# Performance work log

Hardware: AMD Instinct MI355X
Metric: run time of the kernel (lower is better)

## Reference

```python
import jax, jax.numpy as jnp
import numpy as np

BN_EPS = 1e-3  # Keras BatchNormalization default epsilon


def lstm_layer(x, h0, c0, W, U, b):
    # x: [B,T,D]; Keras gate order: i, f, g(cell), o
    def step(carry, xt):
        h, c = carry
        z = xt @ W + h @ U + b               # [B,4H]
        i, f, g, o = jnp.split(z, 4, axis=-1)
        c = jax.nn.sigmoid(f) * c + jax.nn.sigmoid(i) * jnp.tanh(g)
        h = jax.nn.sigmoid(o) * jnp.tanh(c)
        return (h, c), h
    (h, c), ys = jax.lax.scan(step, (h0, c0), x.transpose(1, 0, 2))
    return ys.transpose(1, 0, 2), h, c       # [B,T,H], [B,H], [B,H]


def setup_inputs() -> dict:
    key = jax.random.key(0)
    ks = jax.random.split(key, 8)
    B, T, V, D, H = 64, 128, 32000, 256, 1024
    s = 0.05
    return {
        "tokens": jax.random.randint(ks[0], (B, T), 0, V, dtype=jnp.int32),
        "h0": jnp.zeros((B, H), jnp.float32),
        "c0": jnp.zeros((B, H), jnp.float32),
        "emb": jax.random.normal(ks[1], (V, D), jnp.float32) * s,
        "W0": jax.random.normal(ks[2], (D, 4 * H), jnp.float32) * s,
        "U0": jax.random.normal(ks[3], (H, 4 * H), jnp.float32) * s,
        "b0": jnp.zeros((4 * H,), jnp.float32),
        "W1": jax.random.normal(ks[4], (H, 4 * H), jnp.float32) * s,
        "U1": jax.random.normal(ks[5], (H, 4 * H), jnp.float32) * s,
        "b1": jnp.zeros((4 * H,), jnp.float32),
        "gamma": jnp.ones((H,), jnp.float32),
        "beta": jnp.zeros((H,), jnp.float32),
        "mov_mean": jnp.zeros((H,), jnp.float32),
        "mov_var": jnp.ones((H,), jnp.float32),
    }


def reference(tokens, h0, c0, emb, W0, U0, b0, W1, U1, b1, gamma, beta, mov_mean, mov_var):
    x = emb[tokens]                                   # [B,T,D] embedding lookup
    # Original call() feeds the SAME `hidden` as initial state of layer 0,
    # then the (h,c) of layer 0 as initial state of layer 1 — replicate that.
    x, h, c = lstm_layer(x, h0, c0, W0, U0, b0)
    out, h, c = lstm_layer(x, h, c, W1, U1, b1)
    # BatchNormalization at inference (dropout inactive, moving stats used)
    inv = jax.lax.rsqrt(mov_var + BN_EPS)
    norm = (out - mov_mean) * inv * gamma + beta
    return norm, h, c
```

## Files before the change

kernel.cpp:

```cpp
#include <hip/hip_runtime.h>
#include <hip/hip_bf16.h>


typedef __attribute__((ext_vector_type(8))) short short8;
typedef __attribute__((ext_vector_type(4))) short short4v;
typedef __attribute__((ext_vector_type(4))) float f32x4;
typedef __attribute__((ext_vector_type(16))) float f32x16;
typedef unsigned short ushort_t;

__device__ __forceinline__ void lgkm0_bar() {
  asm volatile("s_waitcnt lgkmcnt(0)" ::: "memory");
  __builtin_amdgcn_s_barrier();
}

__device__ __forceinline__ ushort_t f2b(float f) {
  __hip_bfloat16 h = __float2bfloat16(f);
  return *reinterpret_cast<ushort_t*>(&h);
}
__device__ __forceinline__ float b2f(ushort_t u) {
  unsigned int x = ((unsigned int)u) << 16;
  return __builtin_bit_cast(float, x);
}
__device__ __forceinline__ float fsigmoid(float x) {
  return 1.f / (1.f + __expf(-x));
}
__device__ __forceinline__ float ftanh(float x) {
  return 1.f - 2.f / (__expf(2.f * x) + 1.f);
}

__device__ __forceinline__ void gload_lds16(const ushort_t* g, ushort_t* l) {
  __builtin_amdgcn_global_load_lds(
      (const __attribute__((address_space(1))) unsigned int*)g,
      (__attribute__((address_space(3))) unsigned int*)l, 16, 0, 0);
}

__global__ __launch_bounds__(256) void k_convert(
    const float* __restrict__ src, ushort_t* __restrict__ dst, int kshift) {
  size_t tid = (size_t)blockIdx.x * 256 + threadIdx.x;
  int k = (int)(tid >> 12);
  int c = (int)(tid & 4095);
  int pc = ((c & 1023) << 2) | (c >> 10);
  dst[((size_t)pc << kshift) + k] = f2b(src[tid]);
}

__global__ __launch_bounds__(256) void k_convert_u(
    const float* __restrict__ src, ushort_t* __restrict__ dst) {
  int cid = blockIdx.x * 256 + threadIdx.x;
  int l = cid & 63;
  int ks = (cid >> 6) & 15;
  int kh = (cid >> 10) & 3;
  int ws = cid >> 12;
  int pc = ws * 32 + (l & 31);
  int c = ((pc & 3) << 10) | (pc >> 2);
  int k0 = kh * 256 + ks * 16 + (l >> 5) * 8;
  short8 v;
#pragma unroll
  for (int e = 0; e < 8; ++e)
    v[e] = (short)f2b(src[(size_t)(k0 + e) * 4096 + c]);
  *(short8*)(dst + (size_t)cid * 8) = v;
}

__global__ __launch_bounds__(256) void k_bias(
    const float* __restrict__ b0, const float* __restrict__ b1,
    float* __restrict__ bp0, float* __restrict__ bp1) {
  int pc = blockIdx.x * 256 + threadIdx.x;
  int c = ((pc & 3) << 10) | (pc >> 2);
  bp0[pc] = b0[c];
  bp1[pc] = b1[c];
}

__global__ __launch_bounds__(256) void k_gather(
    const int* __restrict__ tokens, const float* __restrict__ emb,
    ushort_t* __restrict__ Xef) {
  int row = blockIdx.x;
  int t = row >> 6, b = row & 63;
  int tok = tokens[b * 128 + t];
  int d = threadIdx.x;
  Xef[(size_t)row * 256 + d] = f2b(emb[(size_t)tok * 256 + d]);
}

__global__ __launch_bounds__(256) void k_init(
    const float* __restrict__ h0, const float* __restrict__ c0,
    ushort_t* __restrict__ hall, float* __restrict__ c_st,
    unsigned* __restrict__ bars) {
  int tid = blockIdx.x * 256 + threadIdx.x;
  c_st[tid] = c0[tid];
  hall[tid] = f2b(h0[tid]);
  if (tid < 512) bars[tid] = 0;
}

template <int NKS, int LAY>
__global__ __launch_bounds__(256) void k_gemm(
    const ushort_t* __restrict__ Af, const ushort_t* __restrict__ BT,
    ushort_t* __restrict__ C) {
  const int K = NKS * 16;
  const int xcd = blockIdx.x & 7, loc = blockIdx.x >> 3;
  const int wgM = xcd * 8 + (loc & 7);
  const int wgN = loc >> 3;
  const int tid = threadIdx.x;
  const int l = tid & 63;
  const int wv = tid >> 6;
  const int wvM = wv & 1, wvN = wv >> 1;

  __shared__ __align__(16) ushort_t Alds[4096];
  __shared__ __align__(16) ushort_t Blds[4096];

  const int m0 = wgM * 128, n0 = wgN * 128;
  f32x4 acc[4][4] = {};

  for (int k0 = 0; k0 < K; k0 += 32) {
    __syncthreads();
#pragma unroll
    for (int jj = 0; jj < 2; ++jj) {
      int c = jj * 256 + tid;
      int kc = c >> 7, r = c & 127;
      int R = m0 + r;
      int kcg = (k0 >> 3) + kc;
      const ushort_t* asrc =
          (LAY == 0) ? (Af + (size_t)R * 256 + kcg * 8)
                     : (Af + (size_t)(R >> 6) * 65536 + (R & 63) * 1024 + kcg * 8);
      gload_lds16(asrc, (ushort_t*)&Alds[(size_t)(jj * 256 + (tid & ~63)) * 8]);
      gload_lds16(BT + (size_t)(n0 + r) * K + k0 + kc * 8,
                  (ushort_t*)&Blds[(size_t)(jj * 256 + (tid & ~63)) * 8]);
    }
    __syncthreads();

    short8 af[4], bf[4];
#pragma unroll
    for (int mt = 0; mt < 4; ++mt)
      af[mt] = *(const short8*)&Alds[((l >> 4) * 128 + wvM * 64 + mt * 16 + (l & 15)) * 8];
#pragma unroll
    for (int nt = 0; nt < 4; ++nt)
      bf[nt] = *(const short8*)&Blds[((l >> 4) * 128 + wvN * 64 + nt * 16 + (l & 15)) * 8];
#pragma unroll
    for (int mt = 0; mt < 4; ++mt)
#pragma unroll
      for (int nt = 0; nt < 4; ++nt)
        acc[mt][nt] =
            __builtin_amdgcn_mfma_f32_16x16x32_bf16(af[mt], bf[nt], acc[mt][nt], 0, 0, 0);
  }

  const int rr0 = wgM * 128 + wvM * 64 + (l >> 4) * 4;
  const int cc0 = wgN * 128 + wvN * 64 + (l & 15);
#pragma unroll
  for (int mt = 0; mt < 4; ++mt)
#pragma unroll
    for (int nt = 0; nt < 4; ++nt)
#pragma unroll
      for (int r = 0; r < 4; ++r)
        C[(size_t)(rr0 + mt * 16 + r) * 4096 + cc0 + nt * 16] =
            f2b(acc[mt][nt][r]);
}

template <int LAYER>
__global__ __launch_bounds__(256, 1) void k_pers(
    const ushort_t* __restrict__ Uf,
    const ushort_t* __restrict__ XW,
    const float* __restrict__ bp,
    ushort_t* __restrict__ hall,
    float* __restrict__ c_st,
    float* __restrict__ outp,
    const float* __restrict__ gamma, const float* __restrict__ beta,
    const float* __restrict__ mean, const float* __restrict__ var,
    unsigned* __restrict__ bar) {
  const int bid = blockIdx.x;
  const int xcd = bid & 7;
  const int g = xcd & 1;
  const int ws = (xcd >> 1) * 32 + (bid >> 3);
  const int tid = threadIdx.x;
  const int l = tid & 63;
  const int kh = tid >> 6;

  __shared__ __align__(16) ushort_t Ulds[32768];
  __shared__ float zls[4][32][33];
  __shared__ ushort_t hbuf[32][8];

  {
    const ushort_t* src = Uf + (size_t)ws * 32768;
    for (int i = tid; i < 4096; i += 256)
      *(short8*)(Ulds + (size_t)i * 8) = *(const short8*)(src + (size_t)i * 8);
  }

  const int row_o = tid & 31, j_o = tid >> 5;
  const int rowg = g * 32 + row_o;
  const int j = ws * 8 + j_o;
  float creg = c_st[rowg * 1024 + j];
  const f32x4 bias_v = *(const f32x4*)(bp + ws * 32 + j_o * 4);
  float scl = 0.f, sft = 0.f;
  if (LAYER == 1) {
    float inv = rsqrtf(var[j] + 1e-3f);
    scl = inv * gamma[j];
    sft = beta[j] - mean[j] * scl;
  }

  unsigned* grp = bar + xcd * 16;
  unsigned* root = bar + 128 + g * 16;
  const bool leader = (bid >> 3) == 0;

  __syncthreads();

#pragma unroll 1
  for (int t = 0; t < 128; ++t) {
    const ushort_t* hin =
        hall + (size_t)((LAYER == 1 && t == 0) ? 128 : t) * 65536;
    ushort_t* hout = hall + (size_t)(t + 1) * 65536;

    const ushort_t* ab =
        hin + (size_t)(g * 32 + (l & 31)) * 1024 + kh * 256 + (l >> 5) * 8;
    short8 ar[16];
#pragma unroll
    for (int ks = 0; ks < 16; ++ks)
      ar[ks] = *(const short8*)(ab + ks * 16);

    short4v xw = *(const short4v*)(
        XW + ((size_t)(t * 64 + rowg) << 12) + ws * 32 + j_o * 4);

    const ushort_t* uB = Ulds + (size_t)kh * 8192;
    f32x16 acc0 = {}, acc1 = {}, acc2 = {}, acc3 = {};
#pragma unroll
    for (int ks = 0; ks < 16; ks += 4) {
      short8 b0 = *(const short8*)(uB + (size_t)(ks + 0) * 512 + l * 8);
      short8 b1 = *(const short8*)(uB + (size_t)(ks + 1) * 512 + l * 8);
      short8 b2 = *(const short8*)(uB + (size_t)(ks + 2) * 512 + l * 8);
      short8 b3 = *(const short8*)(uB + (size_t)(ks + 3) * 512 + l * 8);
      acc0 = __builtin_amdgcn_mfma_f32_32x32x16_bf16(ar[ks + 0], b0, acc0, 0, 0, 0);
      acc1 = __builtin_amdgcn_mfma_f32_32x32x16_bf16(ar[ks + 1], b1, acc1, 0, 0, 0);
      acc2 = __builtin_amdgcn_mfma_f32_32x32x16_bf16(ar[ks + 2], b2, acc2, 0, 0, 0);
      acc3 = __builtin_amdgcn_mfma_f32_32x32x16_bf16(ar[ks + 3], b3, acc3, 0, 0, 0);
    }
    f32x16 zt = (acc0 + acc1) + (acc2 + acc3);

#pragma unroll
    for (int r = 0; r < 16; ++r)
      zls[kh][(r & 3) + 8 * (r >> 2) + 4 * (l >> 5)][l & 31] = zt[r];
    lgkm0_bar();

    float z4[4];
#pragma unroll
    for (int gi = 0; gi < 4; ++gi) {
      int c = j_o * 4 + gi;
      z4[gi] = ((zls[0][row_o][c] + zls[1][row_o][c]) +
                (zls[2][row_o][c] + zls[3][row_o][c])) +
               b2f((ushort_t)xw[gi]) + bias_v[gi];
    }
    float ii = fsigmoid(z4[0]), ff = fsigmoid(z4[1]);
    float gg = ftanh(z4[2]), oo = fsigmoid(z4[3]);
    creg = ff * creg + ii * gg;
    float hn = oo * ftanh(creg);
    hbuf[row_o][j_o] = f2b(hn);
    if (LAYER == 1) {
      outp[((size_t)rowg * 128 + t) * 1024 + j] = hn * scl + sft;
      if (t == 127) {
        outp[8388608 + rowg * 1024 + j] = hn;
        outp[8454144 + rowg * 1024 + j] = creg;
      }
    } else if (t == 127) {
      c_st[rowg * 1024 + j] = creg;
    }
    lgkm0_bar();

    if (tid < 32) {
      short8 v = *(const short8*)&hbuf[tid][0];
      union { short8 s; unsigned u[4]; } cv;
      cv.s = v;
      unsigned* dst = (unsigned*)(hout + (size_t)(g * 32 + tid) * 1024 + ws * 8);
#pragma unroll
      for (int wi = 0; wi < 4; ++wi)
        __hip_atomic_store(dst + wi, cv.u[wi], __ATOMIC_RELAXED,
                           __HIP_MEMORY_SCOPE_AGENT);
    }

    asm volatile("s_waitcnt vmcnt(0)" ::: "memory");
    __builtin_amdgcn_s_barrier();
    if (tid == 0) {
      __hip_atomic_fetch_add(grp, 1u, __ATOMIC_RELAXED,
                             __HIP_MEMORY_SCOPE_AGENT);
      if (leader) {
        unsigned tg = 32u * (unsigned)(t + 1);
        while (__hip_atomic_load(grp, __ATOMIC_RELAXED,
                                 __HIP_MEMORY_SCOPE_AGENT) < tg)
          __builtin_amdgcn_s_sleep(1);
        __hip_atomic_fetch_add(root, 1u, __ATOMIC_RELAXED,
                               __HIP_MEMORY_SCOPE_AGENT);
      }
      unsigned tr = 4u * (unsigned)(t + 1);
      while (__hip_atomic_load(root, __ATOMIC_RELAXED,
                               __HIP_MEMORY_SCOPE_AGENT) < tr)
        __builtin_amdgcn_s_sleep(1);
    }
    __builtin_amdgcn_s_barrier();
  }
}

extern "C" void kernel_launch(void* const* d_in, const int* in_sizes, int n_in,
                              void* d_out, int out_size, void* d_ws,
                              size_t ws_size, hipStream_t stream) {
  const int* tokens = (const int*)d_in[0];
  const float* h0 = (const float*)d_in[1];
  const float* c0 = (const float*)d_in[2];
  const float* emb = (const float*)d_in[3];
  const float* W0 = (const float*)d_in[4];
  const float* U0 = (const float*)d_in[5];
  const float* b0 = (const float*)d_in[6];
  const float* W1 = (const float*)d_in[7];
  const float* U1 = (const float*)d_in[8];
  const float* b1 = (const float*)d_in[9];
  const float* gammap = (const float*)d_in[10];
  const float* betap = (const float*)d_in[11];
  const float* mmean = (const float*)d_in[12];
  const float* mvar = (const float*)d_in[13];

  char* ws = (char*)d_ws;
  ushort_t* Uc0 = (ushort_t*)(ws + 0);
  ushort_t* Uc1 = (ushort_t*)(ws + 8388608);
  ushort_t* W0f = (ushort_t*)(ws + 16777216);
  ushort_t* W1f = (ushort_t*)(ws + 18874368);
  float* bp0 = (float*)(ws + 27262976);
  float* bp1 = (float*)(ws + 27279360);
  ushort_t* Xef = (ushort_t*)(ws + 27295744);
  ushort_t* XW = (ushort_t*)(ws + 31490048);
  ushort_t* hall = (ushort_t*)(ws + 98598912);
  float* c_st = (float*)(ws + 115507200);
  unsigned* bars = (unsigned*)(ws + 115769344);

  k_convert_u<<<2048, 256, 0, stream>>>(U0, Uc0);
  k_convert_u<<<2048, 256, 0, stream>>>(U1, Uc1);
  k_convert<<<4096, 256, 0, stream>>>(W0, W0f, 8);
  k_convert<<<16384, 256, 0, stream>>>(W1, W1f, 10);
  k_bias<<<16, 256, 0, stream>>>(b0, b1, bp0, bp1);
  k_gather<<<8192, 256, 0, stream>>>(tokens, emb, Xef);
  k_init<<<256, 256, 0, stream>>>(h0, c0, hall, c_st, bars);

  float* outp = (float*)d_out;

  k_gemm<16, 0><<<2048, 256, 0, stream>>>(Xef, W0f, XW);
  k_pers<0><<<256, 256, 0, stream>>>(Uc0, XW, bp0, hall, c_st, nullptr,
                                     nullptr, nullptr, nullptr, nullptr,
                                     bars);

  k_gemm<64, 1><<<2048, 256, 0, stream>>>(hall + 65536, W1f, XW);
  k_pers<1><<<256, 256, 0, stream>>>(Uc1, XW, bp1, hall, c_st, outp, gammap,
                                     betap, mmean, mvar, bars + 160);
}
```

Baseline: 1.773 ms.

## Halve persistent LSTM blocks, widen per-block U slice, flatten grid barrier

```diff
diff --git a/kernel.cpp b/kernel.cpp
--- a/kernel.cpp
+++ b/kernel.cpp
@@ -47,12 +47,13 @@
     const float* __restrict__ src, ushort_t* __restrict__ dst) {
   int cid = blockIdx.x * 256 + threadIdx.x;
   int l = cid & 63;
-  int ks = (cid >> 6) & 15;
-  int kh = (cid >> 10) & 3;
-  int ws = cid >> 12;
-  int pc = ws * 32 + (l & 31);
+  int ks = (cid >> 6) & 31;
+  int kh = (cid >> 11) & 1;
+  int nt = (cid >> 12) & 1;
+  int ws = cid >> 13;
+  int pc = ws * 64 + nt * 32 + (l & 31);
   int c = ((pc & 3) << 10) | (pc >> 2);
-  int k0 = kh * 256 + ks * 16 + (l >> 5) * 8;
+  int k0 = kh * 512 + ks * 16 + (l >> 5) * 8;
   short8 v;
 #pragma unroll
   for (int e = 0; e < 8; ++e)
@@ -164,38 +165,41 @@
     const float* __restrict__ mean, const float* __restrict__ var,
     unsigned* __restrict__ bar) {
   const int bid = blockIdx.x;
-  const int xcd = bid & 7;
-  const int g = xcd & 1;
-  const int ws = (xcd >> 1) * 32 + (bid >> 3);
+  const int g = bid & 1;
+  const int ws = bid >> 1;
   const int tid = threadIdx.x;
   const int l = tid & 63;
-  const int kh = tid >> 6;
-
-  __shared__ __align__(16) ushort_t Ulds[32768];
-  __shared__ float zls[4][32][33];
-  __shared__ ushort_t hbuf[32][8];
+  const int wv = tid >> 6;
+  const int nt = wv & 1, kh = wv >> 1;
+
+  __shared__ __align__(16) ushort_t Ulds[65536];
+  __shared__ float zls[2][2][32][33];
+  __shared__ ushort_t hbuf[32][16];
 
   {
-    const ushort_t* src = Uf + (size_t)ws * 32768;
-    for (int i = tid; i < 4096; i += 256)
+    const ushort_t* src = Uf + (size_t)ws * 65536;
+    for (int i = tid; i < 8192; i += 256)
       *(short8*)(Ulds + (size_t)i * 8) = *(const short8*)(src + (size_t)i * 8);
   }
 
-  const int row_o = tid & 31, j_o = tid >> 5;
+  const int row_o = tid & 31, jp = tid >> 5;
   const int rowg = g * 32 + row_o;
-  const int j = ws * 8 + j_o;
-  float creg = c_st[rowg * 1024 + j];
-  const f32x4 bias_v = *(const f32x4*)(bp + ws * 32 + j_o * 4);
-  float scl = 0.f, sft = 0.f;
-  if (LAYER == 1) {
-    float inv = rsqrtf(var[j] + 1e-3f);
-    scl = inv * gamma[j];
-    sft = beta[j] - mean[j] * scl;
+  float creg[2], scl[2], sft[2];
+#pragma unroll
+  for (int q = 0; q < 2; ++q) {
+    int j = ws * 16 + jp * 2 + q;
+    creg[q] = c_st[rowg * 1024 + j];
+    if (LAYER == 1) {
+      float inv = rsqrtf(var[j] + 1e-3f);
+      scl[q] = inv * gamma[j];
+      sft[q] = beta[j] - mean[j] * scl[q];
+    }
   }
-
-  unsigned* grp = bar + xcd * 16;
-  unsigned* root = bar + 128 + g * 16;
-  const bool leader = (bid >> 3) == 0;
+  const f32x4 bias0 = *(const f32x4*)(bp + ws * 64 + jp * 8);
+  const f32x4 bias1 = *(const f32x4*)(bp + ws * 64 + jp * 8 + 4);
+
+  short8 xwn = *(const short8*)(
+      XW + ((size_t)(0 * 64 + rowg) << 12) + ws * 64 + jp * 8);
 
   __syncthreads();
 
@@ -206,19 +210,16 @@
     ushort_t* hout = hall + (size_t)(t + 1) * 65536;
 
     const ushort_t* ab =
-        hin + (size_t)(g * 32 + (l & 31)) * 1024 + kh * 256 + (l >> 5) * 8;
-    short8 ar[16];
-#pragma unroll
-    for (int ks = 0; ks < 16; ++ks)
+        hin + (size_t)(g * 32 + (l & 31)) * 1024 + kh * 512 + (l >> 5) * 8;
+    short8 ar[32];
+#pragma unroll
+    for (int ks = 0; ks < 32; ++ks)
       ar[ks] = *(const short8*)(ab + ks * 16);
 
-    short4v xw = *(const short4v*)(
-        XW + ((size_t)(t * 64 + rowg) << 12) + ws * 32 + j_o * 4);
-
-    const ushort_t* uB = Ulds + (size_t)kh * 8192;
+    const ushort_t* uB = Ulds + (size_t)(nt * 2 + kh) * 16384;
     f32x16 acc0 = {}, acc1 = {}, acc2 = {}, acc3 = {};
 #pragma unroll
-    for (int ks = 0; ks < 16; ks += 4) {
+    for (int ks = 0; ks < 32; ks += 4) {
       short8 b0 = *(const short8*)(uB + (size_t)(ks + 0) * 512 + l * 8);
       short8 b1 = *(const short8*)(uB + (size_t)(ks + 1) * 512 + l * 8);
       short8 b2 = *(const short8*)(uB + (size_t)(ks + 2) * 512 + l * 8);
@@ -232,38 +233,37 @@
 
 #pragma unroll
     for (int r = 0; r < 16; ++r)
-      zls[kh][(r & 3) + 8 * (r >> 2) + 4 * (l >> 5)][l & 31] = zt[r];
+      zls[kh][nt][(r & 3) + 8 * (r >> 2) + 4 * (l >> 5)][l & 31] = zt[r];
     lgkm0_bar();
 
-    float z4[4];
-#pragma unroll
-    for (int gi = 0; gi < 4; ++gi) {
-      int c = j_o * 4 + gi;
-      z4[gi] = ((zls[0][row_o][c] + zls[1][row_o][c]) +
-                (zls[2][row_o][c] + zls[3][row_o][c])) +
-               b2f((ushort_t)xw[gi]) + bias_v[gi];
-    }
-    float ii = fsigmoid(z4[0]), ff = fsigmoid(z4[1]);
-    float gg = ftanh(z4[2]), oo = fsigmoid(z4[3]);
-    creg = ff * creg + ii * gg;
-    float hn = oo * ftanh(creg);
-    hbuf[row_o][j_o] = f2b(hn);
-    if (LAYER == 1) {
-      outp[((size_t)rowg * 128 + t) * 1024 + j] = hn * scl + sft;
-      if (t == 127) {
-        outp[8388608 + rowg * 1024 + j] = hn;
-        outp[8454144 + rowg * 1024 + j] = creg;
-      }
-    } else if (t == 127) {
-      c_st[rowg * 1024 + j] = creg;
+    float hn2[2];
+#pragma unroll
+    for (int q = 0; q < 2; ++q) {
+      const int j_o = jp * 2 + q;
+      const int nte = j_o >> 3;
+      const int cb = (j_o & 7) * 4;
+      f32x4 zv0 = *(const f32x4*)&zls[0][nte][row_o][cb];
+      f32x4 zv1 = *(const f32x4*)&zls[1][nte][row_o][cb];
+      const f32x4& bv = q ? bias1 : bias0;
+      float zi = zv0[0] + zv1[0] + b2f((ushort_t)xwn[q * 4 + 0]) + bv[0];
+      float zf = zv0[1] + zv1[1] + b2f((ushort_t)xwn[q * 4 + 1]) + bv[1];
+      float zg = zv0[2] + zv1[2] + b2f((ushort_t)xwn[q * 4 + 2]) + bv[2];
+      float zo = zv0[3] + zv1[3] + b2f((ushort_t)xwn[q * 4 + 3]) + bv[3];
+      float ii = fsigmoid(zi), ff = fsigmoid(zf), oo = fsigmoid(zo);
+      float gg = ftanh(zg);
+      creg[q] = ff * creg[q] + ii * gg;
+      hn2[q] = oo * ftanh(creg[q]);
+      hbuf[row_o][j_o] = f2b(hn2[q]);
     }
     lgkm0_bar();
 
-    if (tid < 32) {
-      short8 v = *(const short8*)&hbuf[tid][0];
+    if (tid < 64) {
+      const int row = tid >> 1, half = tid & 1;
+      short8 v = *(const short8*)&hbuf[row][half * 8];
       union { short8 s; unsigned u[4]; } cv;
       cv.s = v;
-      unsigned* dst = (unsigned*)(hout + (size_t)(g * 32 + tid) * 1024 + ws * 8);
+      unsigned* dst =
+          (unsigned*)(hout + (size_t)(g * 32 + row) * 1024 + ws * 16 + half * 8);
 #pragma unroll
       for (int wi = 0; wi < 4; ++wi)
         __hip_atomic_store(dst + wi, cv.u[wi], __ATOMIC_RELAXED,
@@ -271,24 +271,42 @@
     }
 
     asm volatile("s_waitcnt vmcnt(0)" ::: "memory");
-    __builtin_amdgcn_s_barrier();
+    if (tid == 0)
+      __hip_atomic_fetch_add(bar + (bid & 7) * 16, 1u, __ATOMIC_RELAXED,
+                             __HIP_MEMORY_SCOPE_AGENT);
+
+    if (LAYER == 1) {
+#pragma unroll
+      for (int q = 0; q < 2; ++q) {
+        int j = ws * 16 + jp * 2 + q;
+        outp[((size_t)rowg * 128 + t) * 1024 + j] = hn2[q] * scl[q] + sft[q];
+        if (t == 127) {
+          outp[8388608 + rowg * 1024 + j] = hn2[q];
+          outp[8454144 + rowg * 1024 + j] = creg[q];
+        }
+      }
+    } else if (t == 127) {
+#pragma unroll
+      for (int q = 0; q < 2; ++q)
+        c_st[rowg * 1024 + ws * 16 + jp * 2 + q] = creg[q];
+    }
+    if (t < 127)
+      xwn = *(const short8*)(
+          XW + ((size_t)((t + 1) * 64 + rowg) << 12) + ws * 64 + jp * 8);
+
     if (tid == 0) {
-      __hip_atomic_fetch_add(grp, 1u, __ATOMIC_RELAXED,
-                             __HIP_MEMORY_SCOPE_AGENT);
-      if (leader) {
-        unsigned tg = 32u * (unsigned)(t + 1);
-        while (__hip_atomic_load(grp, __ATOMIC_RELAXED,
-                                 __HIP_MEMORY_SCOPE_AGENT) < tg)
-          __builtin_amdgcn_s_sleep(1);
-        __hip_atomic_fetch_add(root, 1u, __ATOMIC_RELAXED,
-                               __HIP_MEMORY_SCOPE_AGENT);
+      const unsigned tgt = 64u * (unsigned)(t + 1);
+      for (;;) {
+        unsigned s = 0;
+#pragma unroll
+        for (int i = 0; i < 4; ++i)
+          s += __hip_atomic_load(bar + (g + 2 * i) * 16, __ATOMIC_RELAXED,
+                                 __HIP_MEMORY_SCOPE_AGENT);
+        if (s >= tgt) break;
+        __builtin_amdgcn_s_sleep(1);
       }
-      unsigned tr = 4u * (unsigned)(t + 1);
-      while (__hip_atomic_load(root, __ATOMIC_RELAXED,
-                               __HIP_MEMORY_SCOPE_AGENT) < tr)
-        __builtin_amdgcn_s_sleep(1);
-    }
-    __builtin_amdgcn_s_barrier();
+    }
+    asm volatile("s_barrier" ::: "memory");
   }
 }
 
@@ -334,11 +352,11 @@
   float* outp = (float*)d_out;
 
   k_gemm<16, 0><<<2048, 256, 0, stream>>>(Xef, W0f, XW);
-  k_pers<0><<<256, 256, 0, stream>>>(Uc0, XW, bp0, hall, c_st, nullptr,
+  k_pers<0><<<128, 256, 0, stream>>>(Uc0, XW, bp0, hall, c_st, nullptr,
                                      nullptr, nullptr, nullptr, nullptr,
                                      bars);
 
   k_gemm<64, 1><<<2048, 256, 0, stream>>>(hall + 65536, W1f, XW);
-  k_pers<1><<<256, 256, 0, stream>>>(Uc1, XW, bp1, hall, c_st, outp, gammap,
-                                     betap, mmean, mvar, bars + 160);
-}
+  k_pers<1><<<128, 256, 0, stream>>>(Uc1, XW, bp1, hall, c_st, outp, gammap,
+                                     betap, mmean, mvar, bars + 128);
+}
```

Measured after the change: 1.815 ms. 1.02x slower.
